# Kernel tuning notes

Measured on AMD Instinct MI355X. Metric: run time of the kernel, lower is better.

Reference implementation:

```python
import jax, jax.numpy as jnp
import numpy as np

T, D, TR, CC, L = 4096, 512, 64, 64, 3  # time, input_size, trace, context, num_blocks


def setup_inputs() -> dict:
    key = jax.random.key(0)
    ks = jax.random.split(key, 10)
    x = jax.random.normal(ks[0], (T, D), dtype=jnp.float32)
    state = jnp.zeros((L, 1, TR, CC), dtype=jnp.float32)  # initial recurrent state (real part; imag is 0)
    start = jax.random.uniform(ks[1], (T,)) < 0.02  # episode-reset mask
    Wtr = jax.random.normal(ks[2], (L, TR, D), dtype=jnp.float32) / np.float32(np.sqrt(D))
    Wc = jax.random.normal(ks[3], (L, TR, D), dtype=jnp.float32) / np.float32(np.sqrt(D))
    a = jax.random.uniform(ks[4], (L, TR), minval=1e-6, maxval=0.1)
    b = 2 * jnp.pi / jnp.exp(jax.random.uniform(ks[5], (L, CC), minval=0.0, maxval=float(np.log(10000.0))))
    F = 2 * TR * CC
    W0 = jax.random.normal(ks[6], (L, D, F), dtype=jnp.float32) * np.float32(0.01 / np.sqrt(F))  # default_init scale=0.01
    b0 = jnp.zeros((L, D)); g0 = jnp.ones((L, D)); beta0 = jnp.zeros((L, D))
    W1 = jax.random.normal(ks[7], (L, D, D), dtype=jnp.float32) / np.float32(np.sqrt(D))
    b1 = jnp.zeros((L, D)); g1 = jnp.ones((L, D)); beta1 = jnp.zeros((L, D))
    return dict(x=x, state=state, start=start, Wtr=Wtr, Wc=Wc, a=a, b=b,
                W0=W0, b0=b0, g0=g0, beta0=beta0, W1=W1, b1=b1, g1=g1, beta1=beta1)


def _layernorm(z, g, b):
    m = jnp.mean(z, axis=-1, keepdims=True)
    v = jnp.mean((z - m) ** 2, axis=-1, keepdims=True)
    return (z - m) / jnp.sqrt(v + 1e-5) * g + b


def _sffm(x, st0, start, Wtr, Wc, a, b, W0, b0, g0, bb0, W1, b1, g1, bb1):
    t_len = x.shape[0]
    tr = x @ Wtr.T           # [T, TR]
    ct = x @ Wc.T            # [T, CC] (context proj also has trace_size outputs)
    pre = jnp.abs(tr[:, :, None] * ct[:, None, :])            # [T, TR, CC]
    pre = pre / (1e-8 + jnp.sum(pre, axis=(-2, -1), keepdims=True))
    # complex decay per (trace, context) pair: exp((-|a| + i b) * dt)
    ab = (-jnp.abs(a))[:, None] + 1j * b[None, :]             # [TR, CC] complex64

    def combine(carry, inc):
        ps, s, i = carry
        st, xx, j = inc
        s = s * jnp.logical_not(st)                            # reset gating
        dt = (j - i).astype(jnp.float32)[:, None, None]
        new = s * jnp.exp(ab[None] * dt) + xx
        return (jnp.logical_or(st, ps), new, j)

    ts = jnp.arange(t_len + 1, dtype=jnp.int32)
    sb = jnp.concatenate([jnp.zeros((1, 1, 1), bool), start.reshape(t_len, 1, 1)], axis=0)
    xs = jnp.concatenate([st0.astype(jnp.complex64), pre.astype(jnp.complex64)], axis=0)
    _, ns, _ = jax.lax.associative_scan(combine, (sb, xs, ts), axis=0)
    ns = ns[1:]                                                # [T, TR, CC] complex

    s = ns.reshape(t_len, TR * CC)
    mag = jnp.log1p(jnp.abs(s))
    ang = jnp.angle(s)
    scaled = jnp.concatenate([mag * jnp.sin(ang), mag * jnp.cos(ang)], axis=-1)  # [T, 2*TR*CC]
    z = jax.nn.leaky_relu(_layernorm(scaled @ W0.T + b0, g0, bb0))
    z = jax.nn.leaky_relu(_layernorm(z @ W1.T + b1, g1, bb1))
    return z


def reference(x, state, start, Wtr, Wc, a, b, W0, b0, g0, beta0, W1, b1, g1, beta1):
    z = x
    for l in range(L):
        z = _sffm(x, state[l], start, Wtr[l], Wc[l], a[l], b[l],
                  W0[l], b0[l], g0[l], beta0[l], W1[l], b1[l], g1[l], beta1[l])
        x = x + z
    return z  # NSFFM returns the last block's y
```

## Files before the change

kernel.cpp:

```cpp
#include <hip/hip_runtime.h>
#include <hip/hip_bf16.h>
#include <math.h>

#define T_LEN 4096
#define D_DIM 512
#define F_DIM 8192
#define NCHUNK 64
#define CLEN 64

typedef short short8 __attribute__((ext_vector_type(8)));
typedef float f32x4 __attribute__((ext_vector_type(4)));
typedef unsigned short u16;
typedef unsigned int u32;

__device__ inline float wave_sum(float v) {
#pragma unroll
  for (int o = 32; o; o >>= 1) v += __shfl_xor(v, o);
  return v;
}

__device__ inline u16 f2bf_bits(float v) {
  __hip_bfloat16 h = __float2bfloat16(v);
  return *(u16*)&h;
}

__device__ inline void gl_lds16(const void* g, void* l) {
  __builtin_amdgcn_global_load_lds((const __attribute__((address_space(1))) void*)g,
                                   (__attribute__((address_space(3))) void*)l, 16, 0, 0);
}

__global__ void detect_start(const unsigned char* __restrict__ s8, int* __restrict__ mode) {
  __shared__ int found;
  if (threadIdx.x == 0) found = 0;
  __syncthreads();
  for (int i = threadIdx.x; i < 4096; i += 256)
    if ((i & 3) && s8[i]) found = 1;
  __syncthreads();
  if (threadIdx.x == 0) mode[0] = found;
}

__device__ inline int read_start(const unsigned char* s8, const int* s32, int mode, int t) {
  return mode ? (int)s8[t] : s32[t];
}

__global__ void f2bf(const float* __restrict__ s, u16* __restrict__ d, int n) {
  int i = blockIdx.x * 256 + threadIdx.x;
  if (i < n) d[i] = f2bf_bits(s[i]);
}

__global__ void k_w1conv(const float* __restrict__ src, u16* __restrict__ dst, int n) {
  int i = blockIdx.x * 256 + threadIdx.x;
  if (i >= n) return;
  int d = (i >> 9) & 511;
  int e = i & 511;
  dst[(i & ~511) | (e ^ ((d & 7) << 3))] = f2bf_bits(src[i]);
}

__global__ void k_conv(const float* __restrict__ wtr, const float* __restrict__ wc,
                       u16* __restrict__ wcat, const float* __restrict__ w0,
                       u16* __restrict__ w0bf) {
  int i = blockIdx.x * 256 + threadIdx.x;
  if (i < 128 * D_DIM) {
    float v = (i < 64 * D_DIM) ? wtr[i] : wc[i - 64 * D_DIM];
    wcat[i] = f2bf_bits(v);
  }
  int j = i - 128 * D_DIM;
  if (j >= 0 && j < D_DIM * F_DIM) {
    int d = j >> 13, f = j & 8191;
    int r = f >> 7, rem = f & 127;
    int c = rem >> 1, b = rem & 1;
    float v = w0[(size_t)d * 8192 + b * 4096 + r * 64 + c];
    w0bf[(size_t)d * 8192 + (f ^ ((d & 7) << 3))] = f2bf_bits(v);
  }
}

template <int BM, int BN, int WR, int WC>
__global__ __launch_bounds__(256) void gemm_bt(const u16* __restrict__ A,
                                               const u16* __restrict__ B,
                                               float* __restrict__ C, int M, int N, int K) {
  constexpr int BK = 32;
  constexpr int MT = BM / (WR * 16);
  constexpr int NT = BN / (WC * 16);
  constexpr int AG = BM / 64;
  constexpr int BG = BN / 64;
  __shared__ u16 sA[BM * BK];
  __shared__ u16 sB[BN * BK];
  const int m0 = blockIdx.x * BM;
  const int n0 = blockIdx.y * BN;
  const int tid = threadIdx.x;
  const int wave = tid >> 6;
  const int lane = tid & 63;
  const int wr = wave / WC;
  const int wc = wave % WC;
  const int row_l = tid >> 2;
  const int c8 = (tid & 3) << 3;
  const int frow = lane & 15;
  const int fcol = (lane >> 4) << 3;

  f32x4 acc[MT][NT];
#pragma unroll
  for (int i = 0; i < MT; ++i)
#pragma unroll
    for (int j = 0; j < NT; ++j) acc[i][j] = (f32x4){0.f, 0.f, 0.f, 0.f};

  for (int k0 = 0; k0 < K; k0 += BK) {
#pragma unroll
    for (int j = 0; j < AG; ++j) {
      uint4 v = *(const uint4*)(A + (size_t)(m0 + j * 64 + row_l) * K + (k0 + c8));
      *(uint4*)(sA + (j * 64 + row_l) * BK + c8) = v;
    }
#pragma unroll
    for (int j = 0; j < BG; ++j) {
      uint4 v = *(const uint4*)(B + (size_t)(n0 + j * 64 + row_l) * K + (k0 + c8));
      *(uint4*)(sB + (j * 64 + row_l) * BK + c8) = v;
    }
    __syncthreads();
    short8 af[MT], bfr[NT];
#pragma unroll
    for (int i = 0; i < MT; ++i)
      af[i] = *(const short8*)(sA + (wr * MT * 16 + i * 16 + frow) * BK + fcol);
#pragma unroll
    for (int j = 0; j < NT; ++j)
      bfr[j] = *(const short8*)(sB + (wc * NT * 16 + j * 16 + frow) * BK + fcol);
#pragma unroll
    for (int i = 0; i < MT; ++i)
#pragma unroll
      for (int j = 0; j < NT; ++j)
        acc[i][j] = __builtin_amdgcn_mfma_f32_16x16x32_bf16(af[i], bfr[j], acc[i][j], 0, 0, 0);
    __syncthreads();
  }
#pragma unroll
  for (int i = 0; i < MT; ++i) {
    const int rbase = m0 + wr * MT * 16 + i * 16 + ((lane >> 4) << 2);
#pragma unroll
    for (int j = 0; j < NT; ++j) {
      const int col = n0 + wc * NT * 16 + j * 16 + (lane & 15);
#pragma unroll
      for (int rg = 0; rg < 4; ++rg) C[(size_t)(rbase + rg) * N + col] = acc[i][j][rg];
    }
  }
}

__global__ __launch_bounds__(256) void gemm128(const u16* __restrict__ A,
                                               const u16* __restrict__ B,
                                               float* __restrict__ Cp, size_t pstride, int N,
                                               int Ktot) {
  __shared__ u16 sA[128 * 64];
  __shared__ u16 sB[128 * 64];
  const int tid = threadIdx.x;
  const int wave = tid >> 6;
  const int lane = tid & 63;
  const int wr = wave >> 1;
  const int wc = wave & 1;
  const int m0 = blockIdx.x * 128;
  const int n0 = blockIdx.y * 128;
  const int ks = blockIdx.z;
  const int Kper = Ktot / gridDim.z;
  const int kb = ks * Kper;
  const int row_s = tid >> 3;
  const int g8 = (tid & 7) << 3;
  const int frow = lane & 15;
  const int quad = lane >> 4;
  const int sw = frow & 7;

  f32x4 acc[4][4];
#pragma unroll
  for (int i = 0; i < 4; ++i)
#pragma unroll
    for (int j = 0; j < 4; ++j) acc[i][j] = (f32x4){0.f, 0.f, 0.f, 0.f};

  for (int k0 = kb; k0 < kb + Kper; k0 += 64) {
#pragma unroll
    for (int j = 0; j < 4; ++j) {
      gl_lds16(A + (size_t)(m0 + j * 32 + row_s) * Ktot + (k0 + g8), sA + j * 2048 + wave * 512);
      gl_lds16(B + (size_t)(n0 + j * 32 + row_s) * Ktot + (k0 + g8), sB + j * 2048 + wave * 512);
    }
    asm volatile("s_waitcnt vmcnt(0)" ::: "memory");
    __syncthreads();
#pragma unroll
    for (int kk = 0; kk < 2; ++kk) {
      const int gA = (((kk << 2) | quad) ^ sw) << 3;
      short8 af[4], bfr[4];
#pragma unroll
      for (int i = 0; i < 4; ++i)
        af[i] = *(const short8*)(sA + (wr * 64 + i * 16 + frow) * 64 + gA);
#pragma unroll
      for (int j = 0; j < 4; ++j)
        bfr[j] = *(const short8*)(sB + (wc * 64 + j * 16 + frow) * 64 + gA);
#pragma unroll
      for (int i = 0; i < 4; ++i)
#pragma unroll
        for (int j = 0; j < 4; ++j)
          acc[i][j] = __builtin_amdgcn_mfma_f32_16x16x32_bf16(af[i], bfr[j], acc[i][j], 0, 0, 0);
    }
    __syncthreads();
  }
#pragma unroll
  for (int i = 0; i < 4; ++i) {
    const int rbase = m0 + wr * 64 + i * 16 + ((lane >> 4) << 2);
#pragma unroll
    for (int j = 0; j < 4; ++j) {
      const int col = n0 + wc * 64 + j * 16 + (lane & 15);
#pragma unroll
      for (int rg = 0; rg < 4; ++rg)
        Cp[(size_t)ks * pstride + (size_t)(rbase + rg) * N + col] = acc[i][j][rg];
    }
  }
}

__global__ void prep_pq(const float* __restrict__ trct, float* __restrict__ pT,
                        float* __restrict__ q) {
  int t = blockIdx.x;
  int lane = threadIdx.x;
  float tr = trct[t * 128 + lane];
  float ct = trct[t * 128 + 64 + lane];
  float ap = fabsf(tr), aq = fabsf(ct);
  float Sp = wave_sum(ap);
  float Sq = wave_sum(aq);
  float denom = 1e-8f + Sp * Sq;
  pT[lane * T_LEN + t] = ap;
  q[t * 64 + lane] = aq / denom;
}

__global__ void scan_phase1(const float* __restrict__ pT, const float* __restrict__ q,
                            const unsigned char* __restrict__ st8, const int* __restrict__ st32,
                            const int* __restrict__ modep, const float* __restrict__ a,
                            const float* __restrict__ b, float4* __restrict__ chunkbuf) {
  int chunk = blockIdx.x, r = blockIdx.y, c = threadIdx.x;
  int mode = modep[0];
  int t0 = chunk * CLEN;
  float na = -fabsf(a[r]);
  float rho = __expf(na);
  float bb = b[c];
  float er = rho * __cosf(bb), ei = rho * __sinf(bb);
  float pv = pT[r * T_LEN + t0 + c];
  int sv = read_start(st8, st32, mode, t0 + c);
  unsigned long long bal = __ballot(sv != 0);
  float Ar, Ai;
  if (bal) {
    Ar = 0.f; Ai = 0.f;
  } else {
    float mag = __expf(64.f * na);
    float ang = 64.f * bb;
    Ar = mag * __cosf(ang);
    Ai = mag * __sinf(ang);
  }
  int L = bal ? (63 - __builtin_clzll(bal)) : 0;
  float Br = 0.f, Bi = 0.f;
  const float* qrow = q + (size_t)t0 * 64 + c;
  for (int i = L; i < CLEN; ++i) {
    float pre = __shfl(pv, i) * qrow[i * 64];
    float nBr = er * Br - ei * Bi + pre;
    Bi = er * Bi + ei * Br;
    Br = nBr;
  }
  chunkbuf[((size_t)chunk * 64 + r) * 64 + c] = make_float4(Ar, Ai, Br, Bi);
}

__global__ void scan_phase2(const float4* __restrict__ chunkbuf, const float* __restrict__ state,
                            float2* __restrict__ s0buf) {
  int r = blockIdx.x, c = threadIdx.x;
  float Sr = state[r * 64 + c], Si = 0.f;
  for (int k = 0; k < NCHUNK; ++k) {
    s0buf[((size_t)k * 64 + r) * 64 + c] = make_float2(Sr, Si);
    float4 ab = chunkbuf[((size_t)k * 64 + r) * 64 + c];
    float nSr = ab.x * Sr - ab.y * Si + ab.z;
    Si = ab.x * Si + ab.y * Sr + ab.w;
    Sr = nSr;
  }
}

__global__ void scan_phase3(const float* __restrict__ pT, const float* __restrict__ q,
                            const unsigned char* __restrict__ st8, const int* __restrict__ st32,
                            const int* __restrict__ modep, const float* __restrict__ a,
                            const float* __restrict__ b, const float2* __restrict__ s0buf,
                            u32* __restrict__ scaled, int c0) {
  int chunk = c0 + blockIdx.x, r = blockIdx.y, c = threadIdx.x;
  int mode = modep[0];
  int t0 = chunk * CLEN;
  float rho = __expf(-fabsf(a[r]));
  float bb = b[c];
  float er = rho * __cosf(bb), ei = rho * __sinf(bb);
  float pv = pT[r * T_LEN + t0 + c];
  int sv = read_start(st8, st32, mode, t0 + c);
  float2 s0 = s0buf[((size_t)chunk * 64 + r) * 64 + c];
  float Sr = s0.x, Si = s0.y;
  int tl0 = (chunk - c0) * CLEN;
  const float* qrow = q + (size_t)t0 * 64 + c;
  u32* srow = scaled + (size_t)tl0 * 4096;
  const int Ldw = r * 64 + c;
#pragma unroll 4
  for (int i = 0; i < CLEN; ++i) {
    float qt = qrow[i * 64];
    float pt = __shfl(pv, i);
    int st = __shfl(sv, i);
    float pre = pt * qt;
    float cer = st ? 0.f : er;
    float cei = st ? 0.f : ei;
    float nSr = cer * Sr - cei * Si + pre;
    Si = cer * Si + cei * Sr;
    Sr = nSr;
    float m2 = fmaf(Sr, Sr, Si * Si);
    float rsq = rsqrtf(fmaxf(m2, 1e-30f));
    float m = m2 * rsq;
    float sc = __log2f(1.0f + m) * 0.6931471805599453f * rsq;
    u32 pack = ((u32)f2bf_bits(sc * Sr) << 16) | (u32)f2bf_bits(sc * Si);
    srow[(size_t)i * 4096 + (Ldw ^ ((i & 7) << 2))] = pack;
  }
}

__global__ void ln_act(const float* __restrict__ parts, int KS, size_t pstride,
                       const float* __restrict__ bias, const float* __restrict__ gam,
                       const float* __restrict__ bet, u16* __restrict__ zbf,
                       const float* __restrict__ xsrc, float* __restrict__ xdst,
                       u16* __restrict__ xbf_next, float* __restrict__ finout) {
  __shared__ float red[8];
  int t = blockIdx.x, tid = threadIdx.x;
  size_t o = (size_t)t * D_DIM + tid;
  float v0 = bias[tid];
  float v1 = bias[tid + 256];
  for (int ks = 0; ks < KS; ++ks) {
    v0 += parts[(size_t)ks * pstride + o];
    v1 += parts[(size_t)ks * pstride + o + 256];
  }
  float s = wave_sum(v0 + v1);
  if ((tid & 63) == 0) red[tid >> 6] = s;
  __syncthreads();
  float mean = (red[0] + red[1] + red[2] + red[3]) * (1.f / 512.f);
  float d0 = v0 - mean, d1 = v1 - mean;
  float s2 = wave_sum(d0 * d0 + d1 * d1);
  if ((tid & 63) == 0) red[4 + (tid >> 6)] = s2;
  __syncthreads();
  float var = (red[4] + red[5] + red[6] + red[7]) * (1.f / 512.f);
  float rstd = rsqrtf(var + 1e-5f);
  float z0 = d0 * rstd * gam[tid] + bet[tid];
  float z1 = d1 * rstd * gam[tid + 256] + bet[tid + 256];
  z0 = z0 > 0.f ? z0 : 0.01f * z0;
  z1 = z1 > 0.f ? z1 : 0.01f * z1;
  if (zbf) {
    int sw8 = (t & 7) << 3;
    size_t zb = (size_t)t * D_DIM;
    zbf[zb + (tid ^ sw8)] = f2bf_bits(z0);
    zbf[zb + 256 + (tid ^ sw8)] = f2bf_bits(z1);
  }
  if (xdst) {
    float x0 = xsrc[o] + z0, x1 = xsrc[o + 256] + z1;
    xdst[o] = x0; xdst[o + 256] = x1;
    if (xbf_next) { xbf_next[o] = f2bf_bits(x0); xbf_next[o + 256] = f2bf_bits(x1); }
  }
  if (finout) { finout[o] = z0; finout[o + 256] = z1; }
}

__global__ void err_signal(float* __restrict__ out, float code) {
  if (threadIdx.x == 0) out[0] = code;
}

extern "C" void kernel_launch(void* const* d_in, const int* in_sizes, int n_in, void* d_out,
                              int out_size, void* d_ws, size_t ws_size, hipStream_t stream) {
  const float* x_in = (const float*)d_in[0];
  const float* state = (const float*)d_in[1];
  const unsigned char* start8 = (const unsigned char*)d_in[2];
  const int* start32 = (const int*)d_in[2];
  const float* Wtr = (const float*)d_in[3];
  const float* Wc = (const float*)d_in[4];
  const float* a_in = (const float*)d_in[5];
  const float* b_in = (const float*)d_in[6];
  const float* W0 = (const float*)d_in[7];
  const float* b0 = (const float*)d_in[8];
  const float* g0 = (const float*)d_in[9];
  const float* beta0 = (const float*)d_in[10];
  const float* W1 = (const float*)d_in[11];
  const float* b1 = (const float*)d_in[12];
  const float* g1 = (const float*)d_in[13];
  const float* beta1 = (const float*)d_in[14];
  float* out = (float*)d_out;

  char* w = (char*)d_ws;
  auto alloc = [&](size_t bytes) {
    char* ptr = w;
    w += (bytes + 255) & ~(size_t)255;
    return ptr;
  };
  float* x_ws = (float*)alloc(4ull * T_LEN * D_DIM);
  u16* xbf = (u16*)alloc(2ull * T_LEN * D_DIM);
  u16* wcat = (u16*)alloc(2ull * 128 * D_DIM);
  u16* w0bf = (u16*)alloc(2ull * D_DIM * F_DIM);
  u16* w1bf = (u16*)alloc(2ull * 3 * D_DIM * D_DIM);
  float* trct = (float*)alloc(4ull * T_LEN * 128);
  float* pTbuf = (float*)alloc(4ull * T_LEN * 64);
  float* qbuf = (float*)alloc(4ull * T_LEN * 64);
  float4* chunkbuf = (float4*)alloc(16ull * NCHUNK * 64 * 64);
  float2* s0buf = (float2*)alloc(8ull * NCHUNK * 64 * 64);
  u16* z0bf = (u16*)alloc(2ull * T_LEN * D_DIM);
  int* modep = (int*)alloc(256);
  size_t base1 = (size_t)(w - (char*)d_ws);

  if (n_in != 15) {
    err_signal<<<1, 64, 0, stream>>>(out, 9e6f + 1000.f * n_in);
    return;
  }
  const size_t MB = 1ull << 20;
  int KS, nseg;
  if (ws_size >= base1 + 64 * MB + 64 * MB) { KS = 8; nseg = 1; }
  else if (ws_size >= base1 + 32 * MB + 64 * MB) { KS = 4; nseg = 1; }
  else if (ws_size >= base1 + 32 * MB + 32 * MB) { KS = 4; nseg = 2; }
  else if (ws_size >= base1 + 16 * MB + 32 * MB) { KS = 2; nseg = 2; }
  else if (ws_size >= base1 + 16 * MB + 16 * MB) { KS = 2; nseg = 4; }
  else if (ws_size >= base1 + 8 * MB + 16 * MB) { KS = 1; nseg = 4; }
  else {
    err_signal<<<1, 64, 0, stream>>>(out, 9e6f);
    return;
  }
  const int KSw1 = (KS >= 8) ? 4 : ((KS >= 2) ? 2 : 1);
  const int seg_rows = T_LEN / nseg;
  const int seg_chunks = NCHUNK / nseg;
  const size_t pstride = (size_t)T_LEN * D_DIM;
  float* ypart = (float*)alloc(4ull * KS * pstride);
  u16* scaled = (u16*)alloc(2ull * seg_rows * F_DIM);

  detect_start<<<1, 256, 0, stream>>>(start8, modep);
  f2bf<<<(T_LEN * D_DIM) / 256, 256, 0, stream>>>(x_in, xbf, T_LEN * D_DIM);
  k_w1conv<<<(3 * D_DIM * D_DIM) / 256, 256, 0, stream>>>(W1, w1bf, 3 * D_DIM * D_DIM);

  for (int l = 0; l < 3; ++l) {
    const float* Wtr_l = Wtr + (size_t)l * 64 * D_DIM;
    const float* Wc_l = Wc + (size_t)l * 64 * D_DIM;
    const float* a_l = a_in + l * 64;
    const float* b_l = b_in + l * 64;
    const float* W0_l = W0 + (size_t)l * D_DIM * F_DIM;
    const u16* w1bf_l = w1bf + (size_t)l * D_DIM * D_DIM;
    const float* state_l = state + (size_t)l * 64 * 64;
    const float* xsrc = (l == 0) ? x_in : x_ws;

    k_conv<<<(128 * D_DIM + D_DIM * F_DIM) / 256, 256, 0, stream>>>(Wtr_l, Wc_l, wcat, W0_l,
                                                                    w0bf);
    gemm_bt<64, 64, 2, 2><<<dim3(T_LEN / 64, 2), 256, 0, stream>>>(xbf, wcat, trct, T_LEN, 128,
                                                                   D_DIM);
    prep_pq<<<T_LEN, 64, 0, stream>>>(trct, pTbuf, qbuf);
    scan_phase1<<<dim3(NCHUNK, 64), 64, 0, stream>>>(pTbuf, qbuf, start8, start32, modep, a_l,
                                                     b_l, chunkbuf);
    scan_phase2<<<64, 64, 0, stream>>>(chunkbuf, state_l, s0buf);

    for (int h = 0; h < nseg; ++h) {
      scan_phase3<<<dim3(seg_chunks, 64), 64, 0, stream>>>(pTbuf, qbuf, start8, start32, modep,
                                                           a_l, b_l, s0buf, (u32*)scaled,
                                                           h * seg_chunks);
      gemm128<<<dim3(seg_rows / 128, D_DIM / 128, KS), 256, 0, stream>>>(
          scaled, w0bf, ypart + (size_t)h * seg_rows * D_DIM, pstride, D_DIM, F_DIM);
    }
    ln_act<<<T_LEN, 256, 0, stream>>>(ypart, KS, pstride, b0 + l * D_DIM, g0 + l * D_DIM,
                                      beta0 + l * D_DIM, z0bf, nullptr, nullptr, nullptr,
                                      nullptr);
    gemm128<<<dim3(T_LEN / 128, D_DIM / 128, KSw1), 256, 0, stream>>>(z0bf, w1bf_l, ypart,
                                                                      pstride, D_DIM, D_DIM);
    ln_act<<<T_LEN, 256, 0, stream>>>(ypart, KSw1, pstride, b1 + l * D_DIM, g1 + l * D_DIM,
                                      beta1 + l * D_DIM, nullptr, (l < 2) ? xsrc : nullptr,
                                      (l < 2) ? x_ws : nullptr, (l < 2) ? xbf : nullptr,
                                      (l == 2) ? out : nullptr);
  }
}
```

Measured before the change: 557.3 us.

## Store split-K partials in bf16 and use unswizzled gemm_bt for W1 projection

The W0 projection's split-K partial sums are now written as bf16 instead of fp32, halving partial-buffer traffic and workspace, which allows KS=4 with a single segment in less memory. The W1 projection moves from the split-K gemm128 to gemm_bt with a single fp32 output, removing its partial reduction. The W1 conversion and z0 writes drop the XOR swizzle to match gemm_bt's layout. Rounding partials to bf16 before summing adds precision error ahead of the layernorm.

```diff
diff --git a/kernel.cpp b/kernel.cpp
--- a/kernel.cpp
+++ b/kernel.cpp
@@ -24,6 +24,11 @@
   return *(u16*)&h;
 }
 
+__device__ inline float bf2f(u16 u) {
+  u32 x = ((u32)u) << 16;
+  return *(float*)&x;
+}
+
 __device__ inline void gl_lds16(const void* g, void* l) {
   __builtin_amdgcn_global_load_lds((const __attribute__((address_space(1))) void*)g,
                                    (__attribute__((address_space(3))) void*)l, 16, 0, 0);
@@ -46,14 +51,6 @@
 __global__ void f2bf(const float* __restrict__ s, u16* __restrict__ d, int n) {
   int i = blockIdx.x * 256 + threadIdx.x;
   if (i < n) d[i] = f2bf_bits(s[i]);
-}
-
-__global__ void k_w1conv(const float* __restrict__ src, u16* __restrict__ dst, int n) {
-  int i = blockIdx.x * 256 + threadIdx.x;
-  if (i >= n) return;
-  int d = (i >> 9) & 511;
-  int e = i & 511;
-  dst[(i & ~511) | (e ^ ((d & 7) << 3))] = f2bf_bits(src[i]);
 }
 
 __global__ void k_conv(const float* __restrict__ wtr, const float* __restrict__ wc,
@@ -143,7 +140,7 @@
 
 __global__ __launch_bounds__(256) void gemm128(const u16* __restrict__ A,
                                                const u16* __restrict__ B,
-                                               float* __restrict__ Cp, size_t pstride, int N,
+                                               u16* __restrict__ Cp, size_t pstride, int N,
                                                int Ktot) {
   __shared__ u16 sA[128 * 64];
   __shared__ u16 sB[128 * 64];
@@ -203,7 +200,7 @@
       const int col = n0 + wc * 64 + j * 16 + (lane & 15);
 #pragma unroll
       for (int rg = 0; rg < 4; ++rg)
-        Cp[(size_t)ks * pstride + (size_t)(rbase + rg) * N + col] = acc[i][j][rg];
+        Cp[(size_t)ks * pstride + (size_t)(rbase + rg) * N + col] = f2bf_bits(acc[i][j][rg]);
     }
   }
 }
@@ -309,19 +306,17 @@
   }
 }
 
-__global__ void ln_act(const float* __restrict__ parts, int KS, size_t pstride,
-                       const float* __restrict__ bias, const float* __restrict__ gam,
-                       const float* __restrict__ bet, u16* __restrict__ zbf,
-                       const float* __restrict__ xsrc, float* __restrict__ xdst,
-                       u16* __restrict__ xbf_next, float* __restrict__ finout) {
+__global__ void ln_act16(const u16* __restrict__ parts, int KS, size_t pstride,
+                         const float* __restrict__ bias, const float* __restrict__ gam,
+                         const float* __restrict__ bet, u16* __restrict__ zbf) {
   __shared__ float red[8];
   int t = blockIdx.x, tid = threadIdx.x;
   size_t o = (size_t)t * D_DIM + tid;
   float v0 = bias[tid];
   float v1 = bias[tid + 256];
   for (int ks = 0; ks < KS; ++ks) {
-    v0 += parts[(size_t)ks * pstride + o];
-    v1 += parts[(size_t)ks * pstride + o + 256];
+    v0 += bf2f(parts[(size_t)ks * pstride + o]);
+    v1 += bf2f(parts[(size_t)ks * pstride + o + 256]);
   }
   float s = wave_sum(v0 + v1);
   if ((tid & 63) == 0) red[tid >> 6] = s;
@@ -337,18 +332,44 @@
   float z1 = d1 * rstd * gam[tid + 256] + bet[tid + 256];
   z0 = z0 > 0.f ? z0 : 0.01f * z0;
   z1 = z1 > 0.f ? z1 : 0.01f * z1;
-  if (zbf) {
-    int sw8 = (t & 7) << 3;
-    size_t zb = (size_t)t * D_DIM;
-    zbf[zb + (tid ^ sw8)] = f2bf_bits(z0);
-    zbf[zb + 256 + (tid ^ sw8)] = f2bf_bits(z1);
-  }
+  zbf[o] = f2bf_bits(z0);
+  zbf[o + 256] = f2bf_bits(z1);
+}
+
+__global__ void ln_act32(const float* __restrict__ y, const float* __restrict__ bias,
+                         const float* __restrict__ gam, const float* __restrict__ bet,
+                         const float* __restrict__ xsrc, float* __restrict__ xdst,
+                         u16* __restrict__ xbf_next, float* __restrict__ finout) {
+  __shared__ float red[8];
+  int t = blockIdx.x, tid = threadIdx.x;
+  size_t o = (size_t)t * D_DIM + tid;
+  float v0 = y[o] + bias[tid];
+  float v1 = y[o + 256] + bias[tid + 256];
+  float s = wave_sum(v0 + v1);
+  if ((tid & 63) == 0) red[tid >> 6] = s;
+  __syncthreads();
+  float mean = (red[0] + red[1] + red[2] + red[3]) * (1.f / 512.f);
+  float d0 = v0 - mean, d1 = v1 - mean;
+  float s2 = wave_sum(d0 * d0 + d1 * d1);
+  if ((tid & 63) == 0) red[4 + (tid >> 6)] = s2;
+  __syncthreads();
+  float var = (red[4] + red[5] + red[6] + red[7]) * (1.f / 512.f);
+  float rstd = rsqrtf(var + 1e-5f);
+  float z0 = d0 * rstd * gam[tid] + bet[tid];
+  float z1 = d1 * rstd * gam[tid + 256] + bet[tid + 256];
+  z0 = z0 > 0.f ? z0 : 0.01f * z0;
+  z1 = z1 > 0.f ? z1 : 0.01f * z1;
   if (xdst) {
     float x0 = xsrc[o] + z0, x1 = xsrc[o + 256] + z1;
-    xdst[o] = x0; xdst[o + 256] = x1;
-    if (xbf_next) { xbf_next[o] = f2bf_bits(x0); xbf_next[o + 256] = f2bf_bits(x1); }
-  }
-  if (finout) { finout[o] = z0; finout[o + 256] = z1; }
+    xdst[o] = x0;
+    xdst[o + 256] = x1;
+    xbf_next[o] = f2bf_bits(x0);
+    xbf_next[o + 256] = f2bf_bits(x1);
+  }
+  if (finout) {
+    finout[o] = z0;
+    finout[o + 256] = z1;
+  }
 }
 
 __global__ void err_signal(float* __restrict__ out, float code) {
@@ -392,6 +413,7 @@
   float4* chunkbuf = (float4*)alloc(16ull * NCHUNK * 64 * 64);
   float2* s0buf = (float2*)alloc(8ull * NCHUNK * 64 * 64);
   u16* z0bf = (u16*)alloc(2ull * T_LEN * D_DIM);
+  float* ybuf = (float*)alloc(4ull * T_LEN * D_DIM);
   int* modep = (int*)alloc(256);
   size_t base1 = (size_t)(w - (char*)d_ws);
 
@@ -400,27 +422,25 @@
     return;
   }
   const size_t MB = 1ull << 20;
+  const size_t pstride = (size_t)T_LEN * D_DIM;
   int KS, nseg;
-  if (ws_size >= base1 + 64 * MB + 64 * MB) { KS = 8; nseg = 1; }
-  else if (ws_size >= base1 + 32 * MB + 64 * MB) { KS = 4; nseg = 1; }
-  else if (ws_size >= base1 + 32 * MB + 32 * MB) { KS = 4; nseg = 2; }
-  else if (ws_size >= base1 + 16 * MB + 32 * MB) { KS = 2; nseg = 2; }
-  else if (ws_size >= base1 + 16 * MB + 16 * MB) { KS = 2; nseg = 4; }
-  else if (ws_size >= base1 + 8 * MB + 16 * MB) { KS = 1; nseg = 4; }
+  if (ws_size >= base1 + 16 * MB + 64 * MB) { KS = 4; nseg = 1; }
+  else if (ws_size >= base1 + 16 * MB + 32 * MB) { KS = 4; nseg = 2; }
+  else if (ws_size >= base1 + 8 * MB + 32 * MB) { KS = 2; nseg = 2; }
+  else if (ws_size >= base1 + 8 * MB + 16 * MB) { KS = 2; nseg = 4; }
+  else if (ws_size >= base1 + 4 * MB + 16 * MB) { KS = 1; nseg = 4; }
   else {
     err_signal<<<1, 64, 0, stream>>>(out, 9e6f);
     return;
   }
-  const int KSw1 = (KS >= 8) ? 4 : ((KS >= 2) ? 2 : 1);
   const int seg_rows = T_LEN / nseg;
   const int seg_chunks = NCHUNK / nseg;
-  const size_t pstride = (size_t)T_LEN * D_DIM;
-  float* ypart = (float*)alloc(4ull * KS * pstride);
+  u16* ypart = (u16*)alloc(2ull * KS * pstride);
   u16* scaled = (u16*)alloc(2ull * seg_rows * F_DIM);
 
   detect_start<<<1, 256, 0, stream>>>(start8, modep);
   f2bf<<<(T_LEN * D_DIM) / 256, 256, 0, stream>>>(x_in, xbf, T_LEN * D_DIM);
-  k_w1conv<<<(3 * D_DIM * D_DIM) / 256, 256, 0, stream>>>(W1, w1bf, 3 * D_DIM * D_DIM);
+  f2bf<<<(3 * D_DIM * D_DIM) / 256, 256, 0, stream>>>(W1, w1bf, 3 * D_DIM * D_DIM);
 
   for (int l = 0; l < 3; ++l) {
     const float* Wtr_l = Wtr + (size_t)l * 64 * D_DIM;
@@ -448,14 +468,12 @@
       gemm128<<<dim3(seg_rows / 128, D_DIM / 128, KS), 256, 0, stream>>>(
           scaled, w0bf, ypart + (size_t)h * seg_rows * D_DIM, pstride, D_DIM, F_DIM);
     }
-    ln_act<<<T_LEN, 256, 0, stream>>>(ypart, KS, pstride, b0 + l * D_DIM, g0 + l * D_DIM,
-                                      beta0 + l * D_DIM, z0bf, nullptr, nullptr, nullptr,
-                                      nullptr);
-    gemm128<<<dim3(T_LEN / 128, D_DIM / 128, KSw1), 256, 0, stream>>>(z0bf, w1bf_l, ypart,
-                                                                      pstride, D_DIM, D_DIM);
-    ln_act<<<T_LEN, 256, 0, stream>>>(ypart, KSw1, pstride, b1 + l * D_DIM, g1 + l * D_DIM,
-                                      beta1 + l * D_DIM, nullptr, (l < 2) ? xsrc : nullptr,
-                                      (l < 2) ? x_ws : nullptr, (l < 2) ? xbf : nullptr,
-                                      (l == 2) ? out : nullptr);
-  }
-}
+    ln_act16<<<T_LEN, 256, 0, stream>>>(ypart, KS, pstride, b0 + l * D_DIM, g0 + l * D_DIM,
+                                        beta0 + l * D_DIM, z0bf);
+    gemm_bt<64, 64, 2, 2><<<dim3(T_LEN / 64, D_DIM / 64), 256, 0, stream>>>(z0bf, w1bf_l, ybuf,
+                                                                            T_LEN, D_DIM, D_DIM);
+    ln_act32<<<T_LEN, 256, 0, stream>>>(ybuf, b1 + l * D_DIM, g1 + l * D_DIM, beta1 + l * D_DIM,
+                                        (l < 2) ? xsrc : nullptr, (l < 2) ? x_ws : nullptr,
+                                        (l < 2) ? xbf : nullptr, (l == 2) ? out : nullptr);
+  }
+}
```

After: 518.7 us. -6.9%, faster.
